# Performance work log

Measured on AMD Instinct MI355X. Metric: run time of the kernel, lower is better.

Reference implementation:

```python
import jax, jax.numpy as jnp
import numpy as np

B, C, H, W = 4, 192, 56, 56


def setup_inputs() -> dict:
    key = jax.random.key(0)
    k1, k2, k3 = jax.random.split(key, 3)
    x = jax.random.normal(k1, (B, C, H, W), dtype=jnp.float32)
    conv_w = jax.random.normal(k2, (C, 2 * C), dtype=jnp.float32) * (1.0 / np.sqrt(2 * C))
    conv_b = jax.random.normal(k3, (C,), dtype=jnp.float32) * 0.01
    bn_gamma = jnp.ones((C,), dtype=jnp.float32)
    bn_beta = jnp.zeros((C,), dtype=jnp.float32)
    bn_mean = jnp.zeros((C,), dtype=jnp.float32)
    bn_var = jnp.ones((C,), dtype=jnp.float32)
    return {"x": x, "conv_w": conv_w, "conv_b": conv_b, "bn_gamma": bn_gamma,
            "bn_beta": bn_beta, "bn_mean": bn_mean, "bn_var": bn_var, "K": 4}


def reference(x, conv_w, conv_b, bn_gamma, bn_beta, bn_mean, bn_var, K):
    b, c, h, w = x.shape
    shifts_h = list(range(0, h, K))          # rolls along H
    shifts_w = list(range(K, w, K))          # rolls along W
    n = len(shifts_h) + len(shifts_w)
    scale = n ** (-0.5)
    # (B, n, C, H, W): all circularly shifted copies (static shift set)
    rolled = jnp.stack([jnp.roll(x, i, axis=2) for i in shifts_h] +
                       [jnp.roll(x, j, axis=3) for j in shifts_w], axis=1)
    # scores: tanh(scale * x * x_rolled), summed over channels -> (B, n, 1, H, W)
    scores = jnp.tanh(rolled * x[:, None] * scale).sum(axis=2, keepdims=True)
    weights = jax.nn.softmax(scores, axis=1)
    out = (rolled * weights).sum(axis=1)     # (B, C, H, W)
    cat = jnp.concatenate([x, out], axis=1)  # (B, 2C, H, W)
    # 1x1 conv as GEMM over channels
    y = jnp.einsum('bchw,oc->bohw', cat, conv_w) + conv_b[None, :, None, None]
    # BatchNorm2d in eval mode (running stats)
    eps = 1e-5
    inv = bn_gamma / jnp.sqrt(bn_var + eps)
    y = (y - bn_mean[None, :, None, None]) * inv[None, :, None, None] + bn_beta[None, :, None, None]
    return jax.nn.gelu(y, approximate=False)
```

## Files before the change

kernel.cpp:

```cpp
#include <hip/hip_runtime.h>
#include <hip/hip_bf16.h>
#include <math.h>

#define BB 4
#define CC 192
#define HH 56
#define WW 56
#define HWW 3136

typedef __attribute__((ext_vector_type(8))) short short8;
typedef __attribute__((ext_vector_type(4))) float f32x4;

__device__ __forceinline__ unsigned short f2b(float f) {
    __hip_bfloat16 h = __float2bfloat16(f);
    return __builtin_bit_cast(unsigned short, h);
}
__device__ __forceinline__ float b2f(unsigned short u) {
    unsigned int x = ((unsigned int)u) << 16;
    return __builtin_bit_cast(float, x);
}
__device__ __forceinline__ void fma4(float4& a, float w, const float4& x) {
    a.x += w * x.x; a.y += w * x.y; a.z += w * x.z; a.w += w * x.w;
}

__global__ __launch_bounds__(256) void k_transpose(const float* __restrict__ x,
                                                   float* __restrict__ xt) {
    __shared__ float tile[32][33];
    int bx = blockIdx.x, by = blockIdx.y, b = blockIdx.z;
    int tx = threadIdx.x, ty = threadIdx.y;
    int p0 = bx * 32, c0 = by * 32;
#pragma unroll
    for (int i = 0; i < 4; i++) {
        int c = c0 + ty + 8 * i;
        tile[ty + 8 * i][tx] = x[(b * CC + c) * HWW + p0 + tx];
    }
    __syncthreads();
#pragma unroll
    for (int i = 0; i < 4; i++) {
        int p = p0 + ty + 8 * i;
        xt[(b * HWW + p) * CC + c0 + tx] = tile[tx][ty + 8 * i];
    }
}

__global__ __launch_bounds__(256) void k_convw(const float* __restrict__ cw,
                                               unsigned short* __restrict__ cwh,
                                               unsigned short* __restrict__ cwl) {
    int i = blockIdx.x * 256 + threadIdx.x;
    if (i < CC * 2 * CC) {
        float v = cw[i];
        unsigned short hi = f2b(v);
        cwh[i] = hi;
        cwl[i] = f2b(v - b2f(hi));
    }
}

__global__ __launch_bounds__(256) void k_scores(const float* __restrict__ xt,
                                                float* __restrict__ sp) {
    __shared__ float Xs[56 * 100];
    int bid = blockIdx.x, tid = threadIdx.x;
    bool isH = bid < 448;
    int lid = isH ? bid : bid - 448;
    int half = lid & 1;
    int cb = lid >> 1;
    int b = cb / 56, l0 = cb % 56;

    const float* src = xt + (size_t)(b * HWW) * CC + half * 96;
    for (int idx = tid; idx < 56 * 24; idx += 256) {
        int t = idx / 24, cq = idx % 24;
        int pix = isH ? (t * WW + l0) : (l0 * WW + t);
        float4 v = *(const float4*)(src + (size_t)pix * CC + cq * 4);
        *(float4*)&Xs[t * 100 + cq * 4] = v;
    }
    __syncthreads();

    const float K2 = 0.38490017945975050f;
    int nU = isH ? 420 : 364;
    for (int u = tid; u < nU; u += 256) {
        int r = u & 3, p = u >> 2;
        int a, bb;
        if (isH) {
            a = (int)((sqrtf((float)(8 * p + 1)) - 1.0f) * 0.5f);
            bb = p - (a * (a + 1)) / 2;
        } else {
            int ap = (int)((sqrtf((float)(8 * p + 1)) - 1.0f) * 0.5f);
            bb = p - (ap * (ap + 1)) / 2;
            a = ap + 1;
        }
        const float* pA = &Xs[(r + 4 * a) * 100];
        const float* pB = &Xs[(r + 4 * bb) * 100];
        float s0 = 0.f, s1 = 0.f, s2 = 0.f, s3 = 0.f;
#pragma unroll
        for (int q = 0; q < 24; q++) {
            float4 av = *(const float4*)(pA + q * 4);
            float4 bv = *(const float4*)(pB + q * 4);
            s0 += __builtin_amdgcn_rcpf(__expf(av.x * bv.x * K2) + 1.0f);
            s1 += __builtin_amdgcn_rcpf(__expf(av.y * bv.y * K2) + 1.0f);
            s2 += __builtin_amdgcn_rcpf(__expf(av.z * bv.z * K2) + 1.0f);
            s3 += __builtin_amdgcn_rcpf(__expf(av.w * bv.w * K2) + 1.0f);
        }
        float s = 96.0f - 2.0f * (s0 + s1 + s2 + s3);
        int sb = (half * BB + b) * 27;
        if (isH) {
            int i1 = a - bb;
            int h1 = r + 4 * a, h2 = r + 4 * bb;
            sp[(sb + i1) * HWW + h1 * WW + l0] = s;
            if (a != bb) sp[(sb + 14 - i1) * HWW + h2 * WW + l0] = s;
        } else {
            int d = a - bb;
            int w1 = r + 4 * a, w2 = r + 4 * bb;
            sp[(sb + 14 + (d - 1)) * HWW + l0 * WW + w1] = s;
            sp[(sb + 14 + (13 - d)) * HWW + l0 * WW + w2] = s;
        }
    }
}

template <bool IS_H>
__device__ __forceinline__ void acc_body(const float* __restrict__ xt,
                                         const float* __restrict__ sp,
                                         float* __restrict__ outt) {
    __shared__ float Wt[14 * 56];
    int lid = blockIdx.x, tid = threadIdx.x;
    int b = lid / 56, l0 = lid % 56;

    if (tid < 56) {
        int pix = IS_H ? (tid * WW + l0) : (l0 * WW + tid);
        float sc[27], mx = -1e30f;
#pragma unroll
        for (int s = 0; s < 27; s++) {
            float v = sp[((0 * BB + b) * 27 + s) * HWW + pix] +
                      sp[((1 * BB + b) * 27 + s) * HWW + pix];
            sc[s] = v; mx = fmaxf(mx, v);
        }
        float sum = 0.f;
#pragma unroll
        for (int s = 0; s < 27; s++) { sc[s] = __expf(sc[s] - mx); sum += sc[s]; }
        float inv = __builtin_amdgcn_rcpf(sum);
        if (IS_H) {
#pragma unroll
            for (int i = 0; i < 14; i++) Wt[i * 56 + tid] = sc[i] * inv;
        } else {
#pragma unroll
            for (int j = 0; j < 13; j++) Wt[j * 56 + tid] = sc[14 + j] * inv;
        }
    }
    __syncthreads();
    if (tid < 192) {
        int r = tid & 3, q = tid >> 2;
        float4 in[14];
#pragma unroll
        for (int t = 0; t < 14; t++) {
            int pix = IS_H ? ((r + 4 * t) * WW + l0) : (l0 * WW + (r + 4 * t));
            in[t] = *(const float4*)(xt + (size_t)(b * HWW + pix) * CC + q * 4);
        }
        float4 acc[14] = {};
        if (IS_H) {
#pragma unroll
            for (int i = 0; i < 14; i++)
#pragma unroll
                for (int a = 0; a < 14; a++)
                    fma4(acc[a], Wt[i * 56 + (r + 4 * a)], in[(a - i + 14) % 14]);
        } else {
#pragma unroll
            for (int j = 0; j < 13; j++)
#pragma unroll
                for (int a = 0; a < 14; a++)
                    fma4(acc[a], Wt[j * 56 + (r + 4 * a)], in[(a - j - 1 + 14) % 14]);
        }
#pragma unroll
        for (int a = 0; a < 14; a++) {
            int pix = IS_H ? ((r + 4 * a) * WW + l0) : (l0 * WW + (r + 4 * a));
            float* dst = outt + (size_t)(b * HWW + pix) * CC + q * 4;
            if (IS_H) {
                *(float4*)dst = acc[a];
            } else {
                float4 prev = *(const float4*)dst;
                prev.x += acc[a].x; prev.y += acc[a].y;
                prev.z += acc[a].z; prev.w += acc[a].w;
                *(float4*)dst = prev;
            }
        }
    }
}

__global__ __launch_bounds__(256) void k_accH(const float* __restrict__ xt,
                                              const float* __restrict__ sp,
                                              float* __restrict__ outt) {
    acc_body<true>(xt, sp, outt);
}
__global__ __launch_bounds__(256) void k_accW(const float* __restrict__ xt,
                                              const float* __restrict__ sp,
                                              float* __restrict__ outt) {
    acc_body<false>(xt, sp, outt);
}

__global__ __launch_bounds__(256) void k_conv(const float* __restrict__ xt,
                                              const float* __restrict__ outt,
                                              const unsigned short* __restrict__ cwh,
                                              const unsigned short* __restrict__ cwl,
                                              const float* __restrict__ cb,
                                              const float* __restrict__ gma,
                                              const float* __restrict__ bta,
                                              const float* __restrict__ mea,
                                              const float* __restrict__ var,
                                              float* __restrict__ y) {
    __shared__ unsigned short AB[4 * 64 * 72];
    unsigned short* Ah = AB;
    unsigned short* Al = AB + 64 * 72;
    unsigned short* Bh = AB + 2 * 64 * 72;
    unsigned short* Bl = AB + 3 * 64 * 72;
    int bm = blockIdx.x * 64, bn = blockIdx.y * 64;
    int tid = threadIdx.x, lane = tid & 63, wv = tid >> 6;

    f32x4 acc[4] = {{0,0,0,0},{0,0,0,0},{0,0,0,0},{0,0,0,0}};

    for (int kc = 0; kc < 384; kc += 64) {
        const float* base = (kc < CC) ? xt : outt;
        int coff = (kc < CC) ? kc : kc - CC;
#pragma unroll
        for (int r2 = 0; r2 < 2; r2++) {
            int idx = tid + r2 * 256;
            int m = idx >> 3, kq = idx & 7;
            const float* s = base + (size_t)(bm + m) * CC + coff + kq * 8;
            float4 v0 = *(const float4*)s;
            float4 v1 = *(const float4*)(s + 4);
            float v[8] = {v0.x, v0.y, v0.z, v0.w, v1.x, v1.y, v1.z, v1.w};
            unsigned short hi[8], lo[8];
#pragma unroll
            for (int e = 0; e < 8; e++) {
                hi[e] = f2b(v[e]);
                lo[e] = f2b(v[e] - b2f(hi[e]));
            }
            *(short8*)&Ah[m * 72 + kq * 8] = *(short8*)hi;
            *(short8*)&Al[m * 72 + kq * 8] = *(short8*)lo;
            int n = m;
            *(short8*)&Bh[n * 72 + kq * 8] =
                *(const short8*)(cwh + (size_t)(bn + n) * 384 + kc + kq * 8);
            *(short8*)&Bl[n * 72 + kq * 8] =
                *(const short8*)(cwl + (size_t)(bn + n) * 384 + kc + kq * 8);
        }
        __syncthreads();
        int n0 = wv * 16;
        int k8 = lane >> 4;
        int col = lane & 15;
#pragma unroll
        for (int ks = 0; ks < 64; ks += 32) {
            int koff = ks + k8 * 8;
            short8 bfh = *(const short8*)&Bh[(n0 + col) * 72 + koff];
            short8 bfl = *(const short8*)&Bl[(n0 + col) * 72 + koff];
#pragma unroll
            for (int fm = 0; fm < 4; fm++) {
                short8 afh = *(const short8*)&Ah[(fm * 16 + col) * 72 + koff];
                short8 afl = *(const short8*)&Al[(fm * 16 + col) * 72 + koff];
                acc[fm] = __builtin_amdgcn_mfma_f32_16x16x32_bf16(afh, bfh, acc[fm], 0, 0, 0);
                acc[fm] = __builtin_amdgcn_mfma_f32_16x16x32_bf16(afl, bfh, acc[fm], 0, 0, 0);
                acc[fm] = __builtin_amdgcn_mfma_f32_16x16x32_bf16(afh, bfl, acc[fm], 0, 0, 0);
            }
        }
        __syncthreads();
    }

    float* Ds = (float*)AB;
    {
        int col = lane & 15, rowq = lane >> 4;
#pragma unroll
        for (int fm = 0; fm < 4; fm++)
#pragma unroll
            for (int rg = 0; rg < 4; rg++)
                Ds[(fm * 16 + rowq * 4 + rg) * 68 + wv * 16 + col] = acc[fm][rg];
    }
    __syncthreads();
    {
        int o = tid >> 2, mq0 = tid & 3;
        int oo = bn + o;
        float bias = cb[oo];
        float inv  = gma[oo] * rsqrtf(var[oo] + 1e-5f);
        float mean = mea[oo], beta = bta[oo];
        int b = bm / HWW, p0 = bm % HWW;
#pragma unroll
        for (int g = 0; g < 4; g++) {
            int mq = mq0 + g * 4;
            float v[4];
#pragma unroll
            for (int j = 0; j < 4; j++) {
                float t = Ds[(mq * 4 + j) * 68 + o] + bias;
                t = (t - mean) * inv + beta;
                v[j] = 0.5f * t * (1.0f + erff(t * 0.70710678118654752f));
            }
            float4 st; st.x = v[0]; st.y = v[1]; st.z = v[2]; st.w = v[3];
            *(float4*)&y[(size_t)(b * CC + oo) * HWW + p0 + mq * 4] = st;
        }
    }
}

extern "C" void kernel_launch(void* const* d_in, const int* in_sizes, int n_in,
                              void* d_out, int out_size, void* d_ws, size_t ws_size,
                              hipStream_t stream) {
    const float* x   = (const float*)d_in[0];
    const float* cw  = (const float*)d_in[1];
    const float* cb  = (const float*)d_in[2];
    const float* gma = (const float*)d_in[3];
    const float* bta = (const float*)d_in[4];
    const float* mea = (const float*)d_in[5];
    const float* var = (const float*)d_in[6];
    float* out = (float*)d_out;

    float* ws = (float*)d_ws;
    float*          xt   = ws;
    float*          sp   = ws + 2408448;
    float*          outt = ws + 3085824;
    unsigned short* cwh  = (unsigned short*)(ws + 5494272);
    unsigned short* cwl  = (unsigned short*)(ws + 5531136);

    k_transpose<<<dim3(98, 6, 4), dim3(32, 8), 0, stream>>>(x, xt);
    k_convw<<<288, 256, 0, stream>>>(cw, cwh, cwl);
    k_scores<<<896, 256, 0, stream>>>(xt, sp);
    k_accH<<<224, 256, 0, stream>>>(xt, sp, outt);
    k_accW<<<224, 256, 0, stream>>>(xt, sp, outt);
    k_conv<<<dim3(196, 3), 256, 0, stream>>>(xt, outt, cwh, cwl, cb, gma, bta, mea, var, out);
}
```

Measured before the change: 133.1 us.

## Precompute bf16 hi/lo splits, merge H/W accumulation, split scores blocks finer

The transpose and accumulation kernels now write bf16 hi/lo pairs directly, so the conv GEMM loads pre-split operands and no longer converts fp32 per tile. The H and W accumulation kernels are merged into one launch that writes separate outputs. This removes the read-modify-write on the shared output; the GEMM instead runs K=576, with duplicated conv weights for the two attention parts. The scores kernel splits each line into two row-class halves, doubling the block count and halving shared memory per block. In exchange the GEMM does more MFMA work and reads more weight data.

```diff
diff --git a/kernel.cpp b/kernel.cpp
--- a/kernel.cpp
+++ b/kernel.cpp
@@ -24,7 +24,9 @@
 }
 
 __global__ __launch_bounds__(256) void k_transpose(const float* __restrict__ x,
-                                                   float* __restrict__ xt) {
+                                                   float* __restrict__ xt,
+                                                   unsigned short* __restrict__ xth,
+                                                   unsigned short* __restrict__ xtl) {
     __shared__ float tile[32][33];
     int bx = blockIdx.x, by = blockIdx.y, b = blockIdx.z;
     int tx = threadIdx.x, ty = threadIdx.y;
@@ -38,7 +40,12 @@
 #pragma unroll
     for (int i = 0; i < 4; i++) {
         int p = p0 + ty + 8 * i;
-        xt[(b * HWW + p) * CC + c0 + tx] = tile[tx][ty + 8 * i];
+        float v = tile[tx][ty + 8 * i];
+        size_t o = (size_t)(b * HWW + p) * CC + c0 + tx;
+        xt[o] = v;
+        unsigned short hi = f2b(v);
+        xth[o] = hi;
+        xtl[o] = f2b(v - b2f(hi));
     }
 }
 
@@ -46,8 +53,10 @@
                                                unsigned short* __restrict__ cwh,
                                                unsigned short* __restrict__ cwl) {
     int i = blockIdx.x * 256 + threadIdx.x;
-    if (i < CC * 2 * CC) {
-        float v = cw[i];
+    if (i < CC * 576) {
+        int o = i / 576, k = i % 576;
+        int ks = (k >= 384) ? (k - 192) : k;
+        float v = cw[o * 384 + ks];
         unsigned short hi = f2b(v);
         cwh[i] = hi;
         cwl[i] = f2b(v - b2f(hi));
@@ -56,27 +65,31 @@
 
 __global__ __launch_bounds__(256) void k_scores(const float* __restrict__ xt,
                                                 float* __restrict__ sp) {
-    __shared__ float Xs[56 * 100];
+    __shared__ float Xs[28 * 100];
     int bid = blockIdx.x, tid = threadIdx.x;
-    bool isH = bid < 448;
-    int lid = isH ? bid : bid - 448;
+    bool isH = bid < 896;
+    int lid = isH ? bid : bid - 896;
     int half = lid & 1;
-    int cb = lid >> 1;
+    int rp = (lid >> 1) & 1;
+    int cb = lid >> 2;
     int b = cb / 56, l0 = cb % 56;
+    int r0 = rp * 2;
 
     const float* src = xt + (size_t)(b * HWW) * CC + half * 96;
-    for (int idx = tid; idx < 56 * 24; idx += 256) {
-        int t = idx / 24, cq = idx % 24;
-        int pix = isH ? (t * WW + l0) : (l0 * WW + t);
+    for (int idx = tid; idx < 28 * 24; idx += 256) {
+        int t2 = idx / 24, cq = idx % 24;
+        int pi = (r0 + t2 / 14) + 4 * (t2 % 14);
+        int pix = isH ? (pi * WW + l0) : (l0 * WW + pi);
         float4 v = *(const float4*)(src + (size_t)pix * CC + cq * 4);
-        *(float4*)&Xs[t * 100 + cq * 4] = v;
+        *(float4*)&Xs[t2 * 100 + cq * 4] = v;
     }
     __syncthreads();
 
     const float K2 = 0.38490017945975050f;
-    int nU = isH ? 420 : 364;
-    for (int u = tid; u < nU; u += 256) {
-        int r = u & 3, p = u >> 2;
+    int perCls = isH ? 105 : 91;
+    int nI = 2 * perCls;
+    if (tid < nI) {
+        int cls = tid / perCls, p = tid % perCls;
         int a, bb;
         if (isH) {
             a = (int)((sqrtf((float)(8 * p + 1)) - 1.0f) * 0.5f);
@@ -86,8 +99,8 @@
             bb = p - (ap * (ap + 1)) / 2;
             a = ap + 1;
         }
-        const float* pA = &Xs[(r + 4 * a) * 100];
-        const float* pB = &Xs[(r + 4 * bb) * 100];
+        const float* pA = &Xs[(cls * 14 + a) * 100];
+        const float* pB = &Xs[(cls * 14 + bb) * 100];
         float s0 = 0.f, s1 = 0.f, s2 = 0.f, s3 = 0.f;
 #pragma unroll
         for (int q = 0; q < 24; q++) {
@@ -99,6 +112,7 @@
             s3 += __builtin_amdgcn_rcpf(__expf(av.w * bv.w * K2) + 1.0f);
         }
         float s = 96.0f - 2.0f * (s0 + s1 + s2 + s3);
+        int r = r0 + cls;
         int sb = (half * BB + b) * 27;
         if (isH) {
             int i1 = a - bb;
@@ -114,16 +128,20 @@
     }
 }
 
-template <bool IS_H>
-__device__ __forceinline__ void acc_body(const float* __restrict__ xt,
-                                         const float* __restrict__ sp,
-                                         float* __restrict__ outt) {
+__global__ __launch_bounds__(256) void k_acc(const float* __restrict__ xt,
+                                             const float* __restrict__ sp,
+                                             unsigned short* __restrict__ oHh,
+                                             unsigned short* __restrict__ oHl,
+                                             unsigned short* __restrict__ oWh,
+                                             unsigned short* __restrict__ oWl) {
     __shared__ float Wt[14 * 56];
-    int lid = blockIdx.x, tid = threadIdx.x;
+    int bid = blockIdx.x, tid = threadIdx.x;
+    bool isH = bid < 224;
+    int lid = isH ? bid : bid - 224;
     int b = lid / 56, l0 = lid % 56;
 
     if (tid < 56) {
-        int pix = IS_H ? (tid * WW + l0) : (l0 * WW + tid);
+        int pix = isH ? (tid * WW + l0) : (l0 * WW + tid);
         float sc[27], mx = -1e30f;
 #pragma unroll
         for (int s = 0; s < 27; s++) {
@@ -135,7 +153,7 @@
 #pragma unroll
         for (int s = 0; s < 27; s++) { sc[s] = __expf(sc[s] - mx); sum += sc[s]; }
         float inv = __builtin_amdgcn_rcpf(sum);
-        if (IS_H) {
+        if (isH) {
 #pragma unroll
             for (int i = 0; i < 14; i++) Wt[i * 56 + tid] = sc[i] * inv;
         } else {
@@ -149,11 +167,11 @@
         float4 in[14];
 #pragma unroll
         for (int t = 0; t < 14; t++) {
-            int pix = IS_H ? ((r + 4 * t) * WW + l0) : (l0 * WW + (r + 4 * t));
+            int pix = isH ? ((r + 4 * t) * WW + l0) : (l0 * WW + (r + 4 * t));
             in[t] = *(const float4*)(xt + (size_t)(b * HWW + pix) * CC + q * 4);
         }
         float4 acc[14] = {};
-        if (IS_H) {
+        if (isH) {
 #pragma unroll
             for (int i = 0; i < 14; i++)
 #pragma unroll
@@ -166,35 +184,29 @@
                 for (int a = 0; a < 14; a++)
                     fma4(acc[a], Wt[j * 56 + (r + 4 * a)], in[(a - j - 1 + 14) % 14]);
         }
+        unsigned short* dh = isH ? oHh : oWh;
+        unsigned short* dl = isH ? oHl : oWl;
 #pragma unroll
         for (int a = 0; a < 14; a++) {
-            int pix = IS_H ? ((r + 4 * a) * WW + l0) : (l0 * WW + (r + 4 * a));
-            float* dst = outt + (size_t)(b * HWW + pix) * CC + q * 4;
-            if (IS_H) {
-                *(float4*)dst = acc[a];
-            } else {
-                float4 prev = *(const float4*)dst;
-                prev.x += acc[a].x; prev.y += acc[a].y;
-                prev.z += acc[a].z; prev.w += acc[a].w;
-                *(float4*)dst = prev;
-            }
-        }
-    }
-}
-
-__global__ __launch_bounds__(256) void k_accH(const float* __restrict__ xt,
-                                              const float* __restrict__ sp,
-                                              float* __restrict__ outt) {
-    acc_body<true>(xt, sp, outt);
-}
-__global__ __launch_bounds__(256) void k_accW(const float* __restrict__ xt,
-                                              const float* __restrict__ sp,
-                                              float* __restrict__ outt) {
-    acc_body<false>(xt, sp, outt);
-}
-
-__global__ __launch_bounds__(256) void k_conv(const float* __restrict__ xt,
-                                              const float* __restrict__ outt,
+            int pix = isH ? ((r + 4 * a) * WW + l0) : (l0 * WW + (r + 4 * a));
+            size_t o = (size_t)(b * HWW + pix) * CC + q * 4;
+            ushort4 hi4, lo4;
+            hi4.x = f2b(acc[a].x); lo4.x = f2b(acc[a].x - b2f(hi4.x));
+            hi4.y = f2b(acc[a].y); lo4.y = f2b(acc[a].y - b2f(hi4.y));
+            hi4.z = f2b(acc[a].z); lo4.z = f2b(acc[a].z - b2f(hi4.z));
+            hi4.w = f2b(acc[a].w); lo4.w = f2b(acc[a].w - b2f(hi4.w));
+            *(ushort4*)(dh + o) = hi4;
+            *(ushort4*)(dl + o) = lo4;
+        }
+    }
+}
+
+__global__ __launch_bounds__(256) void k_conv(const unsigned short* __restrict__ xth,
+                                              const unsigned short* __restrict__ xtl,
+                                              const unsigned short* __restrict__ oHh,
+                                              const unsigned short* __restrict__ oHl,
+                                              const unsigned short* __restrict__ oWh,
+                                              const unsigned short* __restrict__ oWl,
                                               const unsigned short* __restrict__ cwh,
                                               const unsigned short* __restrict__ cwl,
                                               const float* __restrict__ cb,
@@ -213,30 +225,23 @@
 
     f32x4 acc[4] = {{0,0,0,0},{0,0,0,0},{0,0,0,0},{0,0,0,0}};
 
-    for (int kc = 0; kc < 384; kc += 64) {
-        const float* base = (kc < CC) ? xt : outt;
-        int coff = (kc < CC) ? kc : kc - CC;
+    for (int kc9 = 0; kc9 < 9; kc9++) {
+        const unsigned short* sh;
+        const unsigned short* sl;
+        int coff;
+        if (kc9 < 3)      { sh = xth; sl = xtl; coff = kc9 * 64; }
+        else if (kc9 < 6) { sh = oHh; sl = oHl; coff = (kc9 - 3) * 64; }
+        else              { sh = oWh; sl = oWl; coff = (kc9 - 6) * 64; }
 #pragma unroll
         for (int r2 = 0; r2 < 2; r2++) {
             int idx = tid + r2 * 256;
             int m = idx >> 3, kq = idx & 7;
-            const float* s = base + (size_t)(bm + m) * CC + coff + kq * 8;
-            float4 v0 = *(const float4*)s;
-            float4 v1 = *(const float4*)(s + 4);
-            float v[8] = {v0.x, v0.y, v0.z, v0.w, v1.x, v1.y, v1.z, v1.w};
-            unsigned short hi[8], lo[8];
-#pragma unroll
-            for (int e = 0; e < 8; e++) {
-                hi[e] = f2b(v[e]);
-                lo[e] = f2b(v[e] - b2f(hi[e]));
-            }
-            *(short8*)&Ah[m * 72 + kq * 8] = *(short8*)hi;
-            *(short8*)&Al[m * 72 + kq * 8] = *(short8*)lo;
-            int n = m;
-            *(short8*)&Bh[n * 72 + kq * 8] =
-                *(const short8*)(cwh + (size_t)(bn + n) * 384 + kc + kq * 8);
-            *(short8*)&Bl[n * 72 + kq * 8] =
-                *(const short8*)(cwl + (size_t)(bn + n) * 384 + kc + kq * 8);
+            size_t ao = (size_t)(bm + m) * CC + coff + kq * 8;
+            *(short8*)&Ah[m * 72 + kq * 8] = *(const short8*)(sh + ao);
+            *(short8*)&Al[m * 72 + kq * 8] = *(const short8*)(sl + ao);
+            size_t bo = (size_t)(bn + m) * 576 + kc9 * 64 + kq * 8;
+            *(short8*)&Bh[m * 72 + kq * 8] = *(const short8*)(cwh + bo);
+            *(short8*)&Bl[m * 72 + kq * 8] = *(const short8*)(cwl + bo);
         }
         __syncthreads();
         int n0 = wv * 16;
@@ -307,14 +312,19 @@
     float* ws = (float*)d_ws;
     float*          xt   = ws;
     float*          sp   = ws + 2408448;
-    float*          outt = ws + 3085824;
-    unsigned short* cwh  = (unsigned short*)(ws + 5494272);
-    unsigned short* cwl  = (unsigned short*)(ws + 5531136);
-
-    k_transpose<<<dim3(98, 6, 4), dim3(32, 8), 0, stream>>>(x, xt);
-    k_convw<<<288, 256, 0, stream>>>(cw, cwh, cwl);
-    k_scores<<<896, 256, 0, stream>>>(xt, sp);
-    k_accH<<<224, 256, 0, stream>>>(xt, sp, outt);
-    k_accW<<<224, 256, 0, stream>>>(xt, sp, outt);
-    k_conv<<<dim3(196, 3), 256, 0, stream>>>(xt, outt, cwh, cwl, cb, gma, bta, mea, var, out);
-}
+    unsigned short* xth  = (unsigned short*)(ws + 3085824);
+    unsigned short* xtl  = (unsigned short*)(ws + 4290048);
+    unsigned short* oHh  = (unsigned short*)(ws + 5494272);
+    unsigned short* oHl  = (unsigned short*)(ws + 6698496);
+    unsigned short* oWh  = (unsigned short*)(ws + 7902720);
+    unsigned short* oWl  = (unsigned short*)(ws + 9106944);
+    unsigned short* cwh  = (unsigned short*)(ws + 10311168);
+    unsigned short* cwl  = (unsigned short*)(ws + 10366464);
+
+    k_transpose<<<dim3(98, 6, 4), dim3(32, 8), 0, stream>>>(x, xt, xth, xtl);
+    k_convw<<<432, 256, 0, stream>>>(cw, cwh, cwl);
+    k_scores<<<1792, 256, 0, stream>>>(xt, sp);
+    k_acc<<<448, 256, 0, stream>>>(xt, sp, oHh, oHl, oWh, oWl);
+    k_conv<<<dim3(196, 3), 256, 0, stream>>>(xth, xtl, oHh, oHl, oWh, oWl,
+                                             cwh, cwl, cb, gma, bta, mea, var, out);
+}
```

Measured after the change: 139.3 us. +4.7%, slower.
